# Kernel optimization log

Hardware: AMD Instinct MI355X
Metric: run time of the kernel (lower is better)

Reference implementation:

```python
import jax, jax.numpy as jnp
import numpy as np

L = 3            # max degree for L_in = L_edge = L_out = (0, 3)
B = 1024         # batch (number of edges)
C_IN = 256
C_OUT = 256
NUM_ORDERS = (L + 1) ** 2  # 16


def _build_structure(L):
    """Rebuild the coo_CG sparse structure: nonzeros sorted by (M_out, l1, l2),
    using the CG selection rule m1 + m2 = m for valid triangle triples."""
    triples = {}
    for l1 in range(L + 1):
        for l2 in range(L + 1):
            for l in range(abs(l1 - l2), min(L, l1 + l2) + 1):
                key = (l, l1, l2)
                if key not in triples:
                    triples[key] = len(triples)
    M1, M2, seg1, lind_g, seg2 = [], [], [], [], []
    g = 0
    for l in range(L + 1):
        for m in range(-l, l + 1):
            M = l * l + l + m  # flat order index of (l, m)
            for (lo, l1, l2) in sorted(triples.keys()):
                if lo != l:
                    continue
                cnt = 0
                for m1 in range(-l1, l1 + 1):
                    m2 = m - m1
                    if -l2 <= m2 <= l2:
                        M1.append(l1 * l1 + l1 + m1)
                        M2.append(l2 * l2 + l2 + m2)
                        seg1.append(g)
                        cnt += 1
                if cnt > 0:
                    lind_g.append(triples[(lo, l1, l2)])
                    seg2.append(M)
                    g += 1
    return (np.asarray(M1, np.int32), np.asarray(M2, np.int32),
            np.asarray(seg1, np.int32), np.asarray(lind_g, np.int32),
            np.asarray(seg2, np.int32), len(triples), g)


def setup_inputs() -> dict:
    key = jax.random.key(0)
    k1, k2, k3, k4 = jax.random.split(key, 4)
    M1, M2, seg1, l_ind, seg2, n_w, n_g = _build_structure(L)
    # expected: 478 nnz, 156 groups, 34 weights
    x = jax.random.normal(k1, (B, NUM_ORDERS, C_IN), jnp.float32)
    sh = jax.random.normal(k2, (B, NUM_ORDERS), jnp.float32)
    fan = np.sqrt(2.0 / (C_IN + C_OUT)).astype(np.float32)
    weight = jax.random.normal(k3, (n_w, C_IN, C_OUT), jnp.float32) * fan
    CG_vals = jax.random.normal(k4, (M1.shape[0],), jnp.float32) * 0.3
    return {
        'x': x, 'sh': sh, 'weight': weight, 'CG_vals': CG_vals,
        'M1': jnp.asarray(M1), 'M2': jnp.asarray(M2), 'seg1': jnp.asarray(seg1),
        'l_ind': jnp.asarray(l_ind), 'seg2': jnp.asarray(seg2),
        'num_orders_out': NUM_ORDERS,
    }


def reference(x, sh, weight, CG_vals, M1, M2, seg1, l_ind, seg2, num_orders_out):
    # x: (B, Mi, Ci); sh: (B, Me); weight: (num_weights, Ci, Co)
    Bn = x.shape[0]
    G = l_ind.shape[0]
    Ci = x.shape[-1]
    Co = weight.shape[-1]
    feat = x[:, M1, :]                                      # (B, nnz, Ci) gather on orders
    sh_g = sh[:, M2]                                        # (B, nnz)
    inter = (CG_vals[None, :] * sh_g)[..., None] * feat     # (B, nnz, Ci)
    inter = jnp.zeros((Bn, G, Ci), x.dtype).at[:, seg1, :].add(inter)   # segment over (M,l1,l2)
    w = weight[l_ind]                                       # (G, Ci, Co)
    ret = jnp.einsum('bgi,gio->bgo', inter, w)              # per-group matmul
    out = jnp.zeros((Bn, num_orders_out, Co), x.dtype).at[:, seg2, :].add(ret)  # segment over M
    return out
```

## Files before the change

kernel.cpp:

```cpp
#include <hip/hip_runtime.h>
#include <stdint.h>

#define B_SZ 1024
#define NO   16
#define CI   256
#define CO   256
#define BK   64
#define BM   32
#define LDA  72
#define MAXG 12
#define MAXE 48

typedef unsigned short u16;
typedef __attribute__((ext_vector_type(8))) short short8;
typedef __attribute__((ext_vector_type(4))) float f32x4;
typedef __attribute__((ext_vector_type(4))) unsigned short u16x4;
typedef __attribute__((ext_vector_type(8))) unsigned short u16x8;

__device__ __forceinline__ u16 f2bf(float f) {
  union { float f; uint32_t u; } v; v.f = f;
  uint32_t u = v.u;
  return (u16)((u + 0x7FFFu + ((u >> 16) & 1u)) >> 16);
}

__device__ __forceinline__ f32x4 mfma_16x16x32_bf16(short8 a, short8 b, f32x4 c) {
  asm volatile("v_mfma_f32_16x16x32_bf16 %0, %1, %2, %0" : "+v"(c) : "v"(a), "v"(b));
  return c;
}

extern "C" __global__ void wconv_kernel(const float* __restrict__ w,
                                        u16* __restrict__ wbf, int nthreads) {
  int t = blockIdx.x * 256 + threadIdx.x;
  if (t >= nthreads) return;
  int wi  = t >> 13;
  int rem = t & 8191;
  int i8  = (rem & 31) * 8;
  int o   = rem >> 5;
  const float* src = w + (size_t)wi * (CI * CO);
  u16x8 pk;
#pragma unroll
  for (int j = 0; j < 8; ++j) pk[j] = f2bf(src[(size_t)(i8 + j) * CO + o]);
  *(u16x8*)(wbf + (size_t)wi * (CI * CO) + (size_t)o * CI + i8) = pk;
}

extern "C" __global__ void __launch_bounds__(256, 4)
so3_main(const float* __restrict__ x,
         const float* __restrict__ sh,
         const float* __restrict__ CG,
         const u16* __restrict__ wbf,
         const int* __restrict__ M1,
         const int* __restrict__ M2,
         const int* __restrict__ seg1,
         const int* __restrict__ lind,
         const int* __restrict__ seg2,
         float* __restrict__ out,
         int G, int nnz) {
  __shared__ u16 As[BM * LDA];
  __shared__ u16 Bs[128 * LDA];
  __shared__ float coefs[MAXE][BM];
  __shared__ int s_meta[4];
  __shared__ int s_estart[MAXG], s_eend[MAXG], s_wind[MAXG], s_m1[MAXE];

  const int tid = threadIdx.x;
  const int bid = blockIdx.x;
  const int b0  = (bid & 31) * BM;
  const int M   = (bid >> 5) & 15;
  const int co0 = (bid >> 9) * 128;

  if (tid == 0) { s_meta[0] = 1 << 30; s_meta[1] = 0; s_meta[2] = 1 << 30; s_meta[3] = 0; }
  if (tid < MAXG) { s_estart[tid] = 1 << 30; s_eend[tid] = 0; }
  __syncthreads();
  for (int g = tid; g < G; g += 256)
    if (seg2[g] == M) { atomicMin(&s_meta[0], g); atomicMax(&s_meta[1], g + 1); }
  __syncthreads();
  const int gstart = s_meta[0];
  const int ng = s_meta[1] - gstart;
  for (int e = tid; e < nnz; e += 256) {
    int g = seg1[e] - gstart;
    if (g >= 0 && g < ng) {
      atomicMin(&s_meta[2], e); atomicMax(&s_meta[3], e + 1);
      atomicMin(&s_estart[g], e); atomicMax(&s_eend[g], e + 1);
    }
  }
  __syncthreads();
  const int e0 = s_meta[2];
  const int ne = s_meta[3] - e0;
  for (int i = tid; i < ng; i += 256) s_wind[i] = lind[gstart + i];
  for (int i = tid; i < ne; i += 256) s_m1[i] = M1[e0 + i];
  for (int idx = tid; idx < ne * BM; idx += 256) {
    int el = idx / BM, r = idx & (BM - 1);
    int e = e0 + el;
    coefs[el][r] = CG[e] * sh[(size_t)(b0 + r) * NO + M2[e]];
  }
  __syncthreads();

  const int lane = tid & 63;
  const int wave = tid >> 6;
  const int wn = wave;
  const int lrow = lane & 15, lq = lane >> 4;

  f32x4 acc[2][2];
#pragma unroll
  for (int i = 0; i < 2; ++i)
#pragma unroll
    for (int j = 0; j < 2; ++j) acc[i][j] = (f32x4){0.f, 0.f, 0.f, 0.f};

  const int ac  = (tid & 15) * 4;
  const int ar0 = (tid >> 4) * 2;

  for (int gl = 0; gl < ng; ++gl) {
    const int ea = s_estart[gl] - e0;
    const int eb = s_eend[gl] - e0;
    const u16* wb = wbf + (size_t)s_wind[gl] * (CI * CO) + (size_t)co0 * CI;
#pragma unroll 1
    for (int kk = 0; kk < CI; kk += BK) {
#pragma unroll
      for (int r2 = 0; r2 < 2; ++r2) {
        int r = ar0 + r2;
        const float* xrow = x + (size_t)(b0 + r) * (NO * CI) + kk + ac;
        float4 a = make_float4(0.f, 0.f, 0.f, 0.f);
        for (int el = ea; el < eb; ++el) {
          float cf = coefs[el][r];
          float4 xv = *(const float4*)(xrow + s_m1[el] * CI);
          a.x = fmaf(cf, xv.x, a.x); a.y = fmaf(cf, xv.y, a.y);
          a.z = fmaf(cf, xv.z, a.z); a.w = fmaf(cf, xv.w, a.w);
        }
        u16x4 pk; pk[0] = f2bf(a.x); pk[1] = f2bf(a.y); pk[2] = f2bf(a.z); pk[3] = f2bf(a.w);
        *(u16x4*)&As[r * LDA + ac] = pk;
      }
#pragma unroll
      for (int rr = 0; rr < 4; ++rr) {
        int idx = tid + rr * 256;
        int o = idx >> 3, ic = (idx & 7) * 8;
        *(u16x8*)&Bs[o * LDA + ic] = *(const u16x8*)(wb + (size_t)o * CI + kk + ic);
      }
      __syncthreads();
#pragma unroll
      for (int ks = 0; ks < 2; ++ks) {
        short8 af[2], bfr[2];
#pragma unroll
        for (int mf = 0; mf < 2; ++mf)
          af[mf] = *(const short8*)&As[(mf * 16 + lrow) * LDA + ks * 32 + lq * 8];
#pragma unroll
        for (int nf = 0; nf < 2; ++nf)
          bfr[nf] = *(const short8*)&Bs[(wn * 32 + nf * 16 + lrow) * LDA + ks * 32 + lq * 8];
#pragma unroll
        for (int mf = 0; mf < 2; ++mf)
#pragma unroll
          for (int nf = 0; nf < 2; ++nf)
            acc[mf][nf] = mfma_16x16x32_bf16(af[mf], bfr[nf], acc[mf][nf]);
      }
      __syncthreads();
    }
  }

#pragma unroll
  for (int mf = 0; mf < 2; ++mf) {
    int brow = b0 + mf * 16 + lq * 4;
#pragma unroll
    for (int nf = 0; nf < 2; ++nf) {
      int o = co0 + wn * 32 + nf * 16 + lrow;
#pragma unroll
      for (int rg = 0; rg < 4; ++rg)
        out[(size_t)(brow + rg) * (NO * CO) + (size_t)M * CO + o] = acc[mf][nf][rg];
    }
  }
}

extern "C" void kernel_launch(void* const* d_in, const int* in_sizes, int n_in,
                              void* d_out, int out_size, void* d_ws, size_t ws_size,
                              hipStream_t stream) {
  const float* x   = (const float*)d_in[0];
  const float* sh  = (const float*)d_in[1];
  const float* wgt = (const float*)d_in[2];
  const float* CG  = (const float*)d_in[3];
  const int* M1    = (const int*)d_in[4];
  const int* M2    = (const int*)d_in[5];
  const int* seg1  = (const int*)d_in[6];
  const int* lind  = (const int*)d_in[7];
  const int* seg2  = (const int*)d_in[8];
  float* out       = (float*)d_out;

  const int nnz = in_sizes[3];
  const int G   = in_sizes[7];
  const int n_w = in_sizes[2] / (CI * CO);

  u16* wbf = (u16*)d_ws;

  int wthreads = n_w * 8192;
  wconv_kernel<<<dim3((wthreads + 255) / 256), dim3(256), 0, stream>>>(wgt, wbf, wthreads);
  so3_main<<<dim3(1024), dim3(256), 0, stream>>>(x, sh, CG, wbf, M1, M2, seg1, lind, seg2,
                                                 out, G, nnz);
}
```

Baseline: 192.0 us.

## Pre-convert x to bf16, LDS-tiled weight transpose, register-prefetch weight tiles

Adds a pass that converts x to bf16 once, so the main kernel's gather-and-combine reads half the bytes. The weight conversion kernel now transposes through shared memory with coalesced float4 reads in place of strided scalar reads. The main loop is flattened over (group, k-chunk) and prefetches the next weight tile into registers while the current one is computed. The cost is an extra kernel launch plus a full write and read of a bf16 copy of x. Feature products are also now formed from bf16-rounded x, which adds rounding error.

```diff
diff --git a/kernel.cpp b/kernel.cpp
--- a/kernel.cpp
+++ b/kernel.cpp
@@ -10,6 +10,7 @@
 #define LDA  72
 #define MAXG 12
 #define MAXE 48
+#define WP   76
 
 typedef unsigned short u16;
 typedef __attribute__((ext_vector_type(8))) short short8;
@@ -22,29 +23,62 @@
   uint32_t u = v.u;
   return (u16)((u + 0x7FFFu + ((u >> 16) & 1u)) >> 16);
 }
+__device__ __forceinline__ float bf2f(u16 h) {
+  union { float f; uint32_t u; } v; v.u = ((uint32_t)h) << 16; return v.f;
+}
 
 __device__ __forceinline__ f32x4 mfma_16x16x32_bf16(short8 a, short8 b, f32x4 c) {
   asm volatile("v_mfma_f32_16x16x32_bf16 %0, %1, %2, %0" : "+v"(c) : "v"(a), "v"(b));
   return c;
 }
 
+extern "C" __global__ void xconv_kernel(const float* __restrict__ x,
+                                        u16* __restrict__ xbf, int n8) {
+  int t = blockIdx.x * 256 + threadIdx.x;
+  if (t >= n8) return;
+  const float* s = x + (size_t)t * 8;
+  float4 a = ((const float4*)s)[0];
+  float4 b = ((const float4*)s)[1];
+  u16x8 pk;
+  pk[0] = f2bf(a.x); pk[1] = f2bf(a.y); pk[2] = f2bf(a.z); pk[3] = f2bf(a.w);
+  pk[4] = f2bf(b.x); pk[5] = f2bf(b.y); pk[6] = f2bf(b.z); pk[7] = f2bf(b.w);
+  *(u16x8*)(xbf + (size_t)t * 8) = pk;
+}
+
 extern "C" __global__ void wconv_kernel(const float* __restrict__ w,
-                                        u16* __restrict__ wbf, int nthreads) {
-  int t = blockIdx.x * 256 + threadIdx.x;
-  if (t >= nthreads) return;
-  int wi  = t >> 13;
-  int rem = t & 8191;
-  int i8  = (rem & 31) * 8;
-  int o   = rem >> 5;
+                                        u16* __restrict__ wbf) {
+  __shared__ u16 t_lds[64 * WP];
+  const int tid = threadIdx.x;
+  const int bid = blockIdx.x;
+  const int wi = bid >> 4;
+  const int i0 = ((bid >> 2) & 3) * 64;
+  const int o0 = (bid & 3) * 64;
   const float* src = w + (size_t)wi * (CI * CO);
-  u16x8 pk;
-#pragma unroll
-  for (int j = 0; j < 8; ++j) pk[j] = f2bf(src[(size_t)(i8 + j) * CO + o]);
-  *(u16x8*)(wbf + (size_t)wi * (CI * CO) + (size_t)o * CI + i8) = pk;
+  u16* dst = wbf + (size_t)wi * (CI * CO);
+#pragma unroll
+  for (int p = 0; p < 4; ++p) {
+    int idx = p * 256 + tid;
+    int i = idx >> 4, oq = (idx & 15) * 4;
+    float4 v = *(const float4*)(src + (size_t)(i0 + i) * CO + o0 + oq);
+    t_lds[(oq + 0) * WP + i] = f2bf(v.x);
+    t_lds[(oq + 1) * WP + i] = f2bf(v.y);
+    t_lds[(oq + 2) * WP + i] = f2bf(v.z);
+    t_lds[(oq + 3) * WP + i] = f2bf(v.w);
+  }
+  __syncthreads();
+#pragma unroll
+  for (int p = 0; p < 4; ++p) {
+    int idx = p * 256 + tid;
+    int o = idx >> 4, iq = (idx & 15) * 4;
+    u16x4 v;
+    v[0] = t_lds[o * WP + iq + 0]; v[1] = t_lds[o * WP + iq + 1];
+    v[2] = t_lds[o * WP + iq + 2]; v[3] = t_lds[o * WP + iq + 3];
+    *(u16x4*)(dst + (size_t)(o0 + o) * CI + i0 + iq) = v;
+  }
 }
 
 extern "C" __global__ void __launch_bounds__(256, 4)
-so3_main(const float* __restrict__ x,
+so3_main(const u16* __restrict__ xbf,
          const float* __restrict__ sh,
          const float* __restrict__ CG,
          const u16* __restrict__ wbf,
@@ -95,9 +129,10 @@
   __syncthreads();
 
   const int lane = tid & 63;
-  const int wave = tid >> 6;
-  const int wn = wave;
+  const int wn = tid >> 6;
   const int lrow = lane & 15, lq = lane >> 4;
+  const int ar = tid >> 3;
+  const int ak = (tid & 7) * 8;
 
   f32x4 acc[2][2];
 #pragma unroll
@@ -105,53 +140,68 @@
 #pragma unroll
     for (int j = 0; j < 2; ++j) acc[i][j] = (f32x4){0.f, 0.f, 0.f, 0.f};
 
-  const int ac  = (tid & 15) * 4;
-  const int ar0 = (tid >> 4) * 2;
-
-  for (int gl = 0; gl < ng; ++gl) {
-    const int ea = s_estart[gl] - e0;
-    const int eb = s_eend[gl] - e0;
-    const u16* wb = wbf + (size_t)s_wind[gl] * (CI * CO) + (size_t)co0 * CI;
-#pragma unroll 1
-    for (int kk = 0; kk < CI; kk += BK) {
-#pragma unroll
-      for (int r2 = 0; r2 < 2; ++r2) {
-        int r = ar0 + r2;
-        const float* xrow = x + (size_t)(b0 + r) * (NO * CI) + kk + ac;
-        float4 a = make_float4(0.f, 0.f, 0.f, 0.f);
-        for (int el = ea; el < eb; ++el) {
-          float cf = coefs[el][r];
-          float4 xv = *(const float4*)(xrow + s_m1[el] * CI);
-          a.x = fmaf(cf, xv.x, a.x); a.y = fmaf(cf, xv.y, a.y);
-          a.z = fmaf(cf, xv.z, a.z); a.w = fmaf(cf, xv.w, a.w);
-        }
-        u16x4 pk; pk[0] = f2bf(a.x); pk[1] = f2bf(a.y); pk[2] = f2bf(a.z); pk[3] = f2bf(a.w);
-        *(u16x4*)&As[r * LDA + ac] = pk;
+  const int T = ng * 4;
+  u16x8 breg[4];
+  {
+    const u16* wb = wbf + (size_t)s_wind[0] * (CI * CO) + (size_t)co0 * CI;
+#pragma unroll
+    for (int rr = 0; rr < 4; ++rr) {
+      int idx = tid + rr * 256, o = idx >> 3, ic = (idx & 7) * 8;
+      breg[rr] = *(const u16x8*)(wb + (size_t)o * CI + ic);
+    }
+  }
+
+  for (int t = 0; t < T; ++t) {
+    const int gl = t >> 2, kk = (t & 3) * BK;
+    const int ea = s_estart[gl] - e0, eb = s_eend[gl] - e0;
+    {
+      const u16* xrow = xbf + (size_t)(b0 + ar) * (NO * CI) + kk + ak;
+      float ax[8];
+#pragma unroll
+      for (int j = 0; j < 8; ++j) ax[j] = 0.f;
+      for (int el = ea; el < eb; ++el) {
+        float cf = coefs[el][ar];
+        u16x8 xv = *(const u16x8*)(xrow + (size_t)s_m1[el] * CI);
+#pragma unroll
+        for (int j = 0; j < 8; ++j) ax[j] = fmaf(cf, bf2f(xv[j]), ax[j]);
       }
+      u16x8 pk;
+#pragma unroll
+      for (int j = 0; j < 8; ++j) pk[j] = f2bf(ax[j]);
+      *(u16x8*)&As[ar * LDA + ak] = pk;
+    }
+#pragma unroll
+    for (int rr = 0; rr < 4; ++rr) {
+      int idx = tid + rr * 256, o = idx >> 3, ic = (idx & 7) * 8;
+      *(u16x8*)&Bs[o * LDA + ic] = breg[rr];
+    }
+    {
+      int tn = (t + 1 < T) ? t + 1 : t;
+      int gln = tn >> 2, kkn = (tn & 3) * BK;
+      const u16* wbn = wbf + (size_t)s_wind[gln] * (CI * CO) + (size_t)co0 * CI + kkn;
 #pragma unroll
       for (int rr = 0; rr < 4; ++rr) {
-        int idx = tid + rr * 256;
-        int o = idx >> 3, ic = (idx & 7) * 8;
-        *(u16x8*)&Bs[o * LDA + ic] = *(const u16x8*)(wb + (size_t)o * CI + kk + ic);
+        int idx = tid + rr * 256, o = idx >> 3, ic = (idx & 7) * 8;
+        breg[rr] = *(const u16x8*)(wbn + (size_t)o * CI + ic);
       }
-      __syncthreads();
-#pragma unroll
-      for (int ks = 0; ks < 2; ++ks) {
-        short8 af[2], bfr[2];
-#pragma unroll
-        for (int mf = 0; mf < 2; ++mf)
-          af[mf] = *(const short8*)&As[(mf * 16 + lrow) * LDA + ks * 32 + lq * 8];
+    }
+    __syncthreads();
+#pragma unroll
+    for (int ks = 0; ks < 2; ++ks) {
+      short8 af[2], bfr[2];
+#pragma unroll
+      for (int mf = 0; mf < 2; ++mf)
+        af[mf] = *(const short8*)&As[(mf * 16 + lrow) * LDA + ks * 32 + lq * 8];
+#pragma unroll
+      for (int nf = 0; nf < 2; ++nf)
+        bfr[nf] = *(const short8*)&Bs[(wn * 32 + nf * 16 + lrow) * LDA + ks * 32 + lq * 8];
+#pragma unroll
+      for (int mf = 0; mf < 2; ++mf)
 #pragma unroll
         for (int nf = 0; nf < 2; ++nf)
-          bfr[nf] = *(const short8*)&Bs[(wn * 32 + nf * 16 + lrow) * LDA + ks * 32 + lq * 8];
-#pragma unroll
-        for (int mf = 0; mf < 2; ++mf)
-#pragma unroll
-          for (int nf = 0; nf < 2; ++nf)
-            acc[mf][nf] = mfma_16x16x32_bf16(af[mf], bfr[nf], acc[mf][nf]);
-      }
-      __syncthreads();
-    }
+          acc[mf][nf] = mfma_16x16x32_bf16(af[mf], bfr[nf], acc[mf][nf]);
+    }
+    __syncthreads();
   }
 
 #pragma unroll
@@ -185,10 +235,12 @@
   const int G   = in_sizes[7];
   const int n_w = in_sizes[2] / (CI * CO);
 
-  u16* wbf = (u16*)d_ws;
-
-  int wthreads = n_w * 8192;
-  wconv_kernel<<<dim3((wthreads + 255) / 256), dim3(256), 0, stream>>>(wgt, wbf, wthreads);
-  so3_main<<<dim3(1024), dim3(256), 0, stream>>>(x, sh, CG, wbf, M1, M2, seg1, lind, seg2,
+  u16* xbf = (u16*)d_ws;
+  u16* wbf = (u16*)((char*)d_ws + (size_t)B_SZ * NO * CI * 2);
+
+  int n8 = B_SZ * NO * CI / 8;
+  xconv_kernel<<<dim3(n8 / 256), dim3(256), 0, stream>>>(x, xbf, n8);
+  wconv_kernel<<<dim3(n_w * 16), dim3(256), 0, stream>>>(wgt, wbf);
+  so3_main<<<dim3(1024), dim3(256), 0, stream>>>(xbf, sh, CG, wbf, M1, M2, seg1, lind, seg2,
                                                  out, G, nnz);
 }
```

After: 173.1 us. 1.11x faster.
